# Optimization experiments

Hardware: AMD Instinct MI355X
Metric: run time of the kernel (lower is better)

## Reference

```python
import jax, jax.numpy as jnp
import numpy as np

D_MODEL = 512
NUM_HEADS = 8
D_HEAD = D_MODEL // NUM_HEADS


def setup_inputs() -> dict:
    key = jax.random.key(0)
    ks = jax.random.split(key, 9)
    B, L = 4, 2048
    s = 1.0 / np.sqrt(D_MODEL)
    inp = {
        "x": jax.random.normal(ks[0], (B, L, D_MODEL), dtype=jnp.float32),
        "Wq": jax.random.uniform(ks[1], (D_MODEL, D_MODEL), jnp.float32, -s, s),
        "bq": jax.random.uniform(ks[2], (D_MODEL,), jnp.float32, -s, s),
        "Wk": jax.random.uniform(ks[3], (D_MODEL, D_MODEL), jnp.float32, -s, s),
        "bk": jax.random.uniform(ks[4], (D_MODEL,), jnp.float32, -s, s),
        "Wv": jax.random.uniform(ks[5], (D_MODEL, D_MODEL), jnp.float32, -s, s),
        "bv": jax.random.uniform(ks[6], (D_MODEL,), jnp.float32, -s, s),
        "Wo": jax.random.uniform(ks[7], (D_MODEL, D_MODEL), jnp.float32, -s, s),
        "bo": jax.random.uniform(ks[8], (D_MODEL,), jnp.float32, -s, s),
    }
    return inp


def reference(x, Wq, bq, Wk, bk, Wv, bv, Wo, bo):
    B, L, _ = x.shape
    def split_heads(t):  # [B,L,D] -> [B,H,L,d]
        return t.reshape(B, L, NUM_HEADS, D_HEAD).transpose(0, 2, 1, 3)
    Q = split_heads(x @ Wq + bq)
    K = split_heads(x @ Wk + bk)
    V = split_heads(x @ Wv + bv)
    scale = 1.0 / jnp.sqrt(jnp.asarray(D_HEAD, dtype=x.dtype))
    scores = jnp.einsum('bhqd,bhkd->bhqk', Q, K) * scale  # [B,H,L,L]
    weights = jax.nn.softmax(scores, axis=-1)
    z = jnp.einsum('bhqk,bhkd->bhqd', weights, V)  # [B,H,L,d]
    z = z.transpose(0, 2, 1, 3).reshape(B, L, D_MODEL)
    return z @ Wo + bo
```

## Files before the change

### kernel.cpp

```cpp
#include <hip/hip_runtime.h>
#include <hip/hip_bf16.h>
#include <math.h>


#define MDIM 8192
#define DMODEL 512
#define NHEAD 8
#define DHEAD 64
#define LSEQ 2048

typedef __attribute__((ext_vector_type(8))) short short8;
typedef __attribute__((ext_vector_type(4))) float floatx4;

struct alignas(16) bf16x8 { __hip_bfloat16 v[8]; };
struct alignas(8)  bf16x4 { __hip_bfloat16 v[4]; };

__device__ __forceinline__ void load_lds16(const __hip_bfloat16* g, __hip_bfloat16* l) {
    __builtin_amdgcn_global_load_lds(
        (const __attribute__((address_space(1))) void*)g,
        (__attribute__((address_space(3))) void*)l,
        16, 0, 0);
}

__device__ __forceinline__ float fast_exp2(float x) {
#if __has_builtin(__builtin_amdgcn_exp2f)
    return __builtin_amdgcn_exp2f(x);
#else
    return __expf(x * 0.69314718055994531f);
#endif
}

__global__ __launch_bounds__(256) void cast_x_kernel(
    const float* __restrict__ x, __hip_bfloat16* __restrict__ xb)
{
    size_t i = ((size_t)blockIdx.x * 256 + threadIdx.x) * 8;
    float4 a = *reinterpret_cast<const float4*>(x + i);
    float4 b = *reinterpret_cast<const float4*>(x + i + 4);
    bf16x8 o;
    o.v[0] = __float2bfloat16(a.x); o.v[1] = __float2bfloat16(a.y);
    o.v[2] = __float2bfloat16(a.z); o.v[3] = __float2bfloat16(a.w);
    o.v[4] = __float2bfloat16(b.x); o.v[5] = __float2bfloat16(b.y);
    o.v[6] = __float2bfloat16(b.z); o.v[7] = __float2bfloat16(b.w);
    *reinterpret_cast<bf16x8*>(xb + i) = o;
}

__global__ __launch_bounds__(256) void transpose_cast_w(
    const float* __restrict__ Wq, const float* __restrict__ Wk,
    const float* __restrict__ Wv, const float* __restrict__ Wo,
    __hip_bfloat16* __restrict__ Wt)
{
    __shared__ float t[32][33];
    const int z = blockIdx.z;
    const float* W = z == 0 ? Wq : (z == 1 ? Wk : (z == 2 ? Wv : Wo));
    __hip_bfloat16* dst = Wt + ((size_t)z << 18);
    int k0 = blockIdx.x * 32, n0 = blockIdx.y * 32;
    int c = threadIdx.x & 31, r = threadIdx.x >> 5;
    #pragma unroll
    for (int i = 0; i < 4; ++i)
        t[r + 8 * i][c] = W[(size_t)(k0 + r + 8 * i) * DMODEL + n0 + c];
    __syncthreads();
    #pragma unroll
    for (int i = 0; i < 4; ++i)
        dst[(size_t)(n0 + r + 8 * i) * DMODEL + k0 + c] = __float2bfloat16(t[c][r + 8 * i]);
}

__global__ __launch_bounds__(256) void gemm_qkv_mfma(
    const __hip_bfloat16* __restrict__ xb,
    const __hip_bfloat16* __restrict__ Wt,
    const float* __restrict__ bq, const float* __restrict__ bk,
    const float* __restrict__ bv,
    __hip_bfloat16* __restrict__ Q2, __hip_bfloat16* __restrict__ K2,
    __hip_bfloat16* __restrict__ V2)
{
    __shared__ __hip_bfloat16 As[128 * 64];
    __shared__ __hip_bfloat16 Bs[128 * 64];

    const int tid = threadIdx.x;
    const int wid = tid >> 6, lane = tid & 63;
    const int l16 = lane & 15, quad = lane >> 4;
    const int wr = wid >> 1, wc = wid & 1;
    const int row0 = blockIdx.x * 128;
    const int which = blockIdx.y >> 2;
    const int col0 = (blockIdx.y & 3) * 128;
    const __hip_bfloat16* Wb = Wt + ((size_t)which << 18);
    const float* bias = which == 0 ? bq : (which == 1 ? bk : bv);

    const int r8 = lane >> 3, slot = lane & 7;
    const int cchunk = slot ^ (r8 & 7);

    floatx4 acc[4][4];
    #pragma unroll
    for (int i = 0; i < 4; ++i)
        #pragma unroll
        for (int j = 0; j < 4; ++j) acc[i][j] = floatx4{0.f, 0.f, 0.f, 0.f};

    for (int kt = 0; kt < DMODEL / 64; ++kt) {
        __syncthreads();
        #pragma unroll
        for (int j = 0; j < 4; ++j) {
            int seg = wid * 4 + j;
            int m = seg * 8 + r8;
            load_lds16(xb + (size_t)(row0 + m) * DMODEL + kt * 64 + cchunk * 8,
                       As + seg * 512);
            load_lds16(Wb + (size_t)(col0 + m) * DMODEL + kt * 64 + cchunk * 8,
                       Bs + seg * 512);
        }
        __syncthreads();

        #pragma unroll
        for (int ks = 0; ks < 2; ++ks) {
            const int c = ks * 4 + quad;
            short8 af[4], bf[4];
            #pragma unroll
            for (int mt = 0; mt < 4; ++mt) {
                int m = wr * 64 + mt * 16 + l16;
                af[mt] = *reinterpret_cast<const short8*>(As + m * 64 + ((c ^ (m & 7)) << 3));
            }
            #pragma unroll
            for (int nt = 0; nt < 4; ++nt) {
                int n = wc * 64 + nt * 16 + l16;
                bf[nt] = *reinterpret_cast<const short8*>(Bs + n * 64 + ((c ^ (n & 7)) << 3));
            }
            if (which < 2) {
                #pragma unroll
                for (int mt = 0; mt < 4; ++mt)
                    #pragma unroll
                    for (int nt = 0; nt < 4; ++nt)
                        acc[mt][nt] = __builtin_amdgcn_mfma_f32_16x16x32_bf16(
                            bf[nt], af[mt], acc[mt][nt], 0, 0, 0);
            } else {
                #pragma unroll
                for (int mt = 0; mt < 4; ++mt)
                    #pragma unroll
                    for (int nt = 0; nt < 4; ++nt)
                        acc[mt][nt] = __builtin_amdgcn_mfma_f32_16x16x32_bf16(
                            af[mt], bf[nt], acc[mt][nt], 0, 0, 0);
            }
        }
    }

    const float QSCALE = 0.18033688011112042f;

    if (which < 2) {
        __hip_bfloat16* dst = (which == 0) ? Q2 : K2;
        const float sc = (which == 0) ? QSCALE : 1.0f;
        #pragma unroll
        for (int mt = 0; mt < 4; ++mt) {
            const int mm = row0 + wr * 64 + mt * 16 + l16;
            const int b = mm >> 11, l = mm & 2047;
            int rowi;
            if (which == 0) {
                rowi = l;
            } else {
                int hi = l & ~127, w7 = l & 127;
                rowi = hi | (w7 & 96) | (((w7 >> 3) & 3) << 2)
                          | (((w7 >> 2) & 1) << 4) | (w7 & 3);
            }
            #pragma unroll
            for (int nt = 0; nt < 4; ++nt) {
                const int nnb = col0 + wc * 64 + nt * 16 + quad * 4;
                const float4 bv4 = *reinterpret_cast<const float4*>(&bias[nnb]);
                const int h = nnb >> 6, d = nnb & 63;
                const int s = d >> 5, q4 = (d >> 3) & 3, jb = d & 7;
                bf16x4 pk;
                pk.v[0] = __float2bfloat16((acc[mt][nt][0] + bv4.x) * sc);
                pk.v[1] = __float2bfloat16((acc[mt][nt][1] + bv4.y) * sc);
                pk.v[2] = __float2bfloat16((acc[mt][nt][2] + bv4.z) * sc);
                pk.v[3] = __float2bfloat16((acc[mt][nt][3] + bv4.w) * sc);
                size_t idx = ((((size_t)(b * NHEAD + h) * 128 + (rowi >> 4)) * 2 + s) << 9)
                             + q4 * 128 + (rowi & 15) * 8 + jb;
                *reinterpret_cast<bf16x4*>(dst + idx) = pk;
            }
        }
    } else {
        #pragma unroll
        for (int mt = 0; mt < 4; ++mt) {
            const int mmb = row0 + wr * 64 + mt * 16 + quad * 4;
            const int b = mmb >> 11, lb = mmb & 2047;
            #pragma unroll
            for (int nt = 0; nt < 4; ++nt) {
                const int nn = col0 + wc * 64 + nt * 16 + l16;
                const int h = nn >> 6, d = nn & 63;
                const float bv = bias[nn];
                bf16x4 pk;
                pk.v[0] = __float2bfloat16(acc[mt][nt][0] + bv);
                pk.v[1] = __float2bfloat16(acc[mt][nt][1] + bv);
                pk.v[2] = __float2bfloat16(acc[mt][nt][2] + bv);
                pk.v[3] = __float2bfloat16(acc[mt][nt][3] + bv);
                size_t idx = ((((size_t)(b * NHEAD + h) * 64 + (lb >> 5)) * 4 + (d >> 4)) << 9)
                             + ((lb >> 3) & 3) * 128 + (d & 15) * 8 + (lb & 7);
                *reinterpret_cast<bf16x4*>(V2 + idx) = pk;
            }
        }
    }
}

__global__ __launch_bounds__(256) void gemm_out_mfma(
    const __hip_bfloat16* __restrict__ Zb,
    const __hip_bfloat16* __restrict__ WoT,
    const float* __restrict__ bo, float* __restrict__ out)
{
    __shared__ __hip_bfloat16 As[128 * 64];
    __shared__ __hip_bfloat16 Bs[64 * 64];

    const int tid = threadIdx.x;
    const int wid = tid >> 6, lane = tid & 63;
    const int l16 = lane & 15, quad = lane >> 4;
    const int row0 = blockIdx.x * 128;
    const int col0 = blockIdx.y * 64;
    const int r8 = lane >> 3, slot = lane & 7;
    const int cchunk = slot ^ (r8 & 7);

    floatx4 acc[2][4];
    #pragma unroll
    for (int i = 0; i < 2; ++i)
        #pragma unroll
        for (int j = 0; j < 4; ++j) acc[i][j] = floatx4{0.f, 0.f, 0.f, 0.f};

    for (int kt = 0; kt < DMODEL / 64; ++kt) {
        __syncthreads();
        #pragma unroll
        for (int j = 0; j < 4; ++j) {
            int seg = wid * 4 + j;
            int m = seg * 8 + r8;
            load_lds16(Zb + (size_t)(row0 + m) * DMODEL + kt * 64 + cchunk * 8,
                       As + seg * 512);
        }
        #pragma unroll
        for (int j = 0; j < 2; ++j) {
            int seg = wid * 2 + j;
            int n = seg * 8 + r8;
            load_lds16(WoT + (size_t)(col0 + n) * DMODEL + kt * 64 + cchunk * 8,
                       Bs + seg * 512);
        }
        __syncthreads();

        #pragma unroll
        for (int ks = 0; ks < 2; ++ks) {
            const int c = ks * 4 + quad;
            short8 af[2], bf[4];
            #pragma unroll
            for (int mt = 0; mt < 2; ++mt) {
                int m = wid * 32 + mt * 16 + l16;
                af[mt] = *reinterpret_cast<const short8*>(As + m * 64 + ((c ^ (m & 7)) << 3));
            }
            #pragma unroll
            for (int nt = 0; nt < 4; ++nt) {
                int n = nt * 16 + l16;
                bf[nt] = *reinterpret_cast<const short8*>(Bs + n * 64 + ((c ^ (n & 7)) << 3));
            }
            #pragma unroll
            for (int mt = 0; mt < 2; ++mt)
                #pragma unroll
                for (int nt = 0; nt < 4; ++nt)
                    acc[mt][nt] = __builtin_amdgcn_mfma_f32_16x16x32_bf16(
                        af[mt], bf[nt], acc[mt][nt], 0, 0, 0);
        }
    }

    #pragma unroll
    for (int mt = 0; mt < 2; ++mt) {
        const int mmbase = row0 + wid * 32 + mt * 16 + quad * 4;
        #pragma unroll
        for (int nt = 0; nt < 4; ++nt) {
            const int nn = col0 + nt * 16 + l16;
            const float bias_v = bo[nn];
            #pragma unroll
            for (int r = 0; r < 4; ++r)
                out[(size_t)(mmbase + r) * DMODEL + nn] = acc[mt][nt][r] + bias_v;
        }
    }
}

__global__ __launch_bounds__(256) void attn_mfma(
    const __hip_bfloat16* __restrict__ Q2,
    const __hip_bfloat16* __restrict__ K2,
    const __hip_bfloat16* __restrict__ V2,
    __hip_bfloat16* __restrict__ Z)
{
    __shared__ float smem[4608];
    float* Lred = smem;
    float* Ored = smem + 256;

    const int bh = blockIdx.x & 31;
    const int qt = blockIdx.x >> 5;
    const int q0 = qt * 64;
    const int tid = threadIdx.x;
    const int wid = tid >> 6, lane = tid & 63;
    const int l16 = lane & 15, quad = lane >> 4;

    const __hip_bfloat16* Kc = K2 + (((size_t)bh * 128 * 2) << 9);
    const __hip_bfloat16* Vc = V2 + (((size_t)bh * 64 * 4) << 9);

    short8 qb[4][2];
    #pragma unroll
    for (int nt = 0; nt < 4; ++nt)
        #pragma unroll
        for (int s = 0; s < 2; ++s)
            qb[nt][s] = *reinterpret_cast<const short8*>(
                Q2 + ((((size_t)bh * 128 + qt * 4 + nt) * 2 + s) << 9) + lane * 8);

    floatx4 acc[4][4];
    #pragma unroll
    for (int i = 0; i < 4; ++i)
        #pragma unroll
        for (int j = 0; j < 4; ++j) acc[i][j] = floatx4{0.f, 0.f, 0.f, 0.f};
    float lsum[4] = {0.f, 0.f, 0.f, 0.f};

    short8 kb[2][2], vb[4];
    #pragma unroll
    for (int t = 0; t < 2; ++t)
        #pragma unroll
        for (int s = 0; s < 2; ++s)
            kb[t][s] = *reinterpret_cast<const short8*>(
                Kc + ((((size_t)(wid * 2 + t)) * 2 + s) << 9) + lane * 8);
    #pragma unroll
    for (int dt = 0; dt < 4; ++dt)
        vb[dt] = *reinterpret_cast<const short8*>(
            Vc + ((((size_t)wid) * 4 + dt) << 9) + lane * 8);

    for (int kt = 0; kt < LSEQ / 128; ++kt) {
        const int ktn = (kt + 1) & (LSEQ / 128 - 1);
        short8 nkb[2][2], nvb[4];
        #pragma unroll
        for (int t = 0; t < 2; ++t)
            #pragma unroll
            for (int s = 0; s < 2; ++s)
                nkb[t][s] = *reinterpret_cast<const short8*>(
                    Kc + ((((size_t)(ktn * 8 + wid * 2 + t)) * 2 + s) << 9) + lane * 8);
        #pragma unroll
        for (int dt = 0; dt < 4; ++dt)
            nvb[dt] = *reinterpret_cast<const short8*>(
                Vc + ((((size_t)(ktn * 4 + wid)) * 4 + dt) << 9) + lane * 8);

        floatx4 sacc[2][4];
        #pragma unroll
        for (int t = 0; t < 2; ++t)
            #pragma unroll
            for (int nt = 0; nt < 4; ++nt) sacc[t][nt] = floatx4{0.f, 0.f, 0.f, 0.f};
        #pragma unroll
        for (int s = 0; s < 2; ++s) {
            #pragma unroll
            for (int nt = 0; nt < 4; ++nt) {
                sacc[0][nt] = __builtin_amdgcn_mfma_f32_16x16x32_bf16(
                    kb[0][s], qb[nt][s], sacc[0][nt], 0, 0, 0);
                sacc[1][nt] = __builtin_amdgcn_mfma_f32_16x16x32_bf16(
                    kb[1][s], qb[nt][s], sacc[1][nt], 0, 0, 0);
            }
        }

        short8 pa[4];
        #pragma unroll
        for (int nt = 0; nt < 4; ++nt) {
            float e[8];
            #pragma unroll
            for (int t = 0; t < 2; ++t)
                #pragma unroll
                for (int r = 0; r < 4; ++r)
                    e[t * 4 + r] = fast_exp2(sacc[t][nt][r]);
            union { short8 s8; __hip_bfloat16 h[8]; } u;
            #pragma unroll
            for (int i = 0; i < 8; ++i) u.h[i] = __float2bfloat16(e[i]);
            lsum[nt] += ((e[0] + e[1]) + (e[2] + e[3])) + ((e[4] + e[5]) + (e[6] + e[7]));
            pa[nt] = u.s8;
        }

        #pragma unroll
        for (int dt = 0; dt < 4; ++dt)
            #pragma unroll
            for (int nt = 0; nt < 4; ++nt)
                acc[nt][dt] = __builtin_amdgcn_mfma_f32_16x16x32_bf16(
                    pa[nt], vb[dt], acc[nt][dt], 0, 0, 0);

        #pragma unroll
        for (int t = 0; t < 2; ++t)
            #pragma unroll
            for (int s = 0; s < 2; ++s) kb[t][s] = nkb[t][s];
        #pragma unroll
        for (int dt = 0; dt < 4; ++dt) vb[dt] = nvb[dt];
    }

    #pragma unroll
    for (int nt = 0; nt < 4; ++nt) {
        float v = lsum[nt];
        v += __shfl_xor(v, 16);
        v += __shfl_xor(v, 32);
        lsum[nt] = v;
    }
    if (quad == 0) {
        #pragma unroll
        for (int nt = 0; nt < 4; ++nt)
            Lred[wid * 64 + nt * 16 + l16] = lsum[nt];
    }

    const int b = bh >> 3, h = bh & 7;
    const int ql = tid >> 2;
    const int dg = tid & 3;
    float inv = 0.f;

    for (int dt = 0; dt < 4; ++dt) {
        __syncthreads();
        #pragma unroll
        for (int nt = 0; nt < 4; ++nt)
            *reinterpret_cast<floatx4*>(
                &Ored[(wid * 16 + l16) * 68 + nt * 16 + quad * 4]) = acc[nt][dt];
        __syncthreads();

        if (dt == 0)
            inv = 1.f / (Lred[ql] + Lred[64 + ql] + Lred[128 + ql] + Lred[192 + ql]);

        bf16x4 zo;
        #pragma unroll
        for (int i = 0; i < 4; ++i) {
            int d = dg * 4 + i;
            float ssum = Ored[d * 68 + ql] + Ored[(16 + d) * 68 + ql]
                       + Ored[(32 + d) * 68 + ql] + Ored[(48 + d) * 68 + ql];
            zo.v[i] = __float2bfloat16(ssum * inv);
        }
        *reinterpret_cast<bf16x4*>(
            Z + (size_t)(b * LSEQ + q0 + ql) * DMODEL + h * 64 + dt * 16 + dg * 4) = zo;
    }
}

extern "C" void kernel_launch(void* const* d_in, const int* in_sizes, int n_in,
                              void* d_out, int out_size, void* d_ws, size_t ws_size,
                              hipStream_t stream)
{
    const float* x  = (const float*)d_in[0];
    const float* Wq = (const float*)d_in[1]; const float* bq = (const float*)d_in[2];
    const float* Wk = (const float*)d_in[3]; const float* bk = (const float*)d_in[4];
    const float* Wv = (const float*)d_in[5]; const float* bv = (const float*)d_in[6];
    const float* Wo = (const float*)d_in[7]; const float* bo = (const float*)d_in[8];
    float* out = (float*)d_out;

    const size_t nqkv = (size_t)MDIM * DMODEL;
    __hip_bfloat16* xb = (__hip_bfloat16*)d_ws;
    __hip_bfloat16* Wt = xb + nqkv;
    __hip_bfloat16* Q2 = Wt + ((size_t)4 << 18);
    __hip_bfloat16* K2 = Q2 + nqkv;
    __hip_bfloat16* V2 = K2 + nqkv;
    __hip_bfloat16* Zb = V2 + nqkv;

    cast_x_kernel<<<dim3(MDIM * DMODEL / (256 * 8)), 256, 0, stream>>>(x, xb);
    transpose_cast_w<<<dim3(16, 16, 4), 256, 0, stream>>>(Wq, Wk, Wv, Wo, Wt);

    gemm_qkv_mfma<<<dim3(MDIM / 128, 12), 256, 0, stream>>>(
        xb, Wt, bq, bk, bv, Q2, K2, V2);

    attn_mfma<<<dim3(32 * (LSEQ / 64)), 256, 0, stream>>>(Q2, K2, V2, Zb);

    gemm_out_mfma<<<dim3(MDIM / 128, DMODEL / 64), 256, 0, stream>>>(
        Zb, Wt + ((size_t)3 << 18), bo, out);
}
```

Baseline: 159.6 us.

## Compute softmax row sums via MFMA with ones vector, drop register prefetch

Replaces the per-lane float accumulation of exp values and the cross-lane shuffle reduction with an extra MFMA that multiplies the bf16 probabilities by a ones vector, so the matrix unit produces the row sums. It also removes software double-buffering of the K/V fragments in favour of in-loop loads through incrementing pointers, and zero-initialises the score MFMAs through the accumulator operand. The changes cut VALU adds and register pressure but add MFMA work, expose global load latency without explicit prefetch, and sum the bf16-rounded probabilities instead of fp32 ones.

```diff
diff --git a/kernel.cpp b/kernel.cpp
--- a/kernel.cpp
+++ b/kernel.cpp
@@ -305,65 +305,65 @@
     for (int i = 0; i < 4; ++i)
         #pragma unroll
         for (int j = 0; j < 4; ++j) acc[i][j] = floatx4{0.f, 0.f, 0.f, 0.f};
-    float lsum[4] = {0.f, 0.f, 0.f, 0.f};
-
-    short8 kb[2][2], vb[4];
-    #pragma unroll
-    for (int t = 0; t < 2; ++t)
-        #pragma unroll
-        for (int s = 0; s < 2; ++s)
-            kb[t][s] = *reinterpret_cast<const short8*>(
-                Kc + ((((size_t)(wid * 2 + t)) * 2 + s) << 9) + lane * 8);
-    #pragma unroll
-    for (int dt = 0; dt < 4; ++dt)
-        vb[dt] = *reinterpret_cast<const short8*>(
-            Vc + ((((size_t)wid) * 4 + dt) << 9) + lane * 8);
+    floatx4 accl[4];
+    #pragma unroll
+    for (int i = 0; i < 4; ++i) accl[i] = floatx4{0.f, 0.f, 0.f, 0.f};
+
+    union { short8 s8; __hip_bfloat16 h[8]; } onesu;
+    #pragma unroll
+    for (int i = 0; i < 8; ++i) onesu.h[i] = __float2bfloat16(1.0f);
+    const short8 ones = onesu.s8;
+
+    const floatx4 fzero = floatx4{0.f, 0.f, 0.f, 0.f};
+
+    const __hip_bfloat16* kp = Kc + (((size_t)wid * 4) << 9) + lane * 8;
+    const __hip_bfloat16* vp = Vc + (((size_t)wid * 4) << 9) + lane * 8;
 
     for (int kt = 0; kt < LSEQ / 128; ++kt) {
-        const int ktn = (kt + 1) & (LSEQ / 128 - 1);
-        short8 nkb[2][2], nvb[4];
+        short8 kb[2][2], vb[4];
         #pragma unroll
         for (int t = 0; t < 2; ++t)
             #pragma unroll
             for (int s = 0; s < 2; ++s)
-                nkb[t][s] = *reinterpret_cast<const short8*>(
-                    Kc + ((((size_t)(ktn * 8 + wid * 2 + t)) * 2 + s) << 9) + lane * 8);
+                kb[t][s] = *reinterpret_cast<const short8*>(kp + ((t * 2 + s) << 9));
         #pragma unroll
         for (int dt = 0; dt < 4; ++dt)
-            nvb[dt] = *reinterpret_cast<const short8*>(
-                Vc + ((((size_t)(ktn * 4 + wid)) * 4 + dt) << 9) + lane * 8);
+            vb[dt] = *reinterpret_cast<const short8*>(vp + (dt << 9));
+        kp += (size_t)16 << 9;
+        vp += (size_t)16 << 9;
 
         floatx4 sacc[2][4];
         #pragma unroll
-        for (int t = 0; t < 2; ++t)
-            #pragma unroll
-            for (int nt = 0; nt < 4; ++nt) sacc[t][nt] = floatx4{0.f, 0.f, 0.f, 0.f};
-        #pragma unroll
-        for (int s = 0; s < 2; ++s) {
-            #pragma unroll
-            for (int nt = 0; nt < 4; ++nt) {
-                sacc[0][nt] = __builtin_amdgcn_mfma_f32_16x16x32_bf16(
-                    kb[0][s], qb[nt][s], sacc[0][nt], 0, 0, 0);
-                sacc[1][nt] = __builtin_amdgcn_mfma_f32_16x16x32_bf16(
-                    kb[1][s], qb[nt][s], sacc[1][nt], 0, 0, 0);
-            }
+        for (int nt = 0; nt < 4; ++nt) {
+            sacc[0][nt] = __builtin_amdgcn_mfma_f32_16x16x32_bf16(
+                kb[0][0], qb[nt][0], fzero, 0, 0, 0);
+            sacc[1][nt] = __builtin_amdgcn_mfma_f32_16x16x32_bf16(
+                kb[1][0], qb[nt][0], fzero, 0, 0, 0);
+        }
+        #pragma unroll
+        for (int nt = 0; nt < 4; ++nt) {
+            sacc[0][nt] = __builtin_amdgcn_mfma_f32_16x16x32_bf16(
+                kb[0][1], qb[nt][1], sacc[0][nt], 0, 0, 0);
+            sacc[1][nt] = __builtin_amdgcn_mfma_f32_16x16x32_bf16(
+                kb[1][1], qb[nt][1], sacc[1][nt], 0, 0, 0);
         }
 
         short8 pa[4];
         #pragma unroll
         for (int nt = 0; nt < 4; ++nt) {
-            float e[8];
+            union { short8 s8; __hip_bfloat16 h[8]; } u;
             #pragma unroll
             for (int t = 0; t < 2; ++t)
                 #pragma unroll
                 for (int r = 0; r < 4; ++r)
-                    e[t * 4 + r] = fast_exp2(sacc[t][nt][r]);
-            union { short8 s8; __hip_bfloat16 h[8]; } u;
-            #pragma unroll
-            for (int i = 0; i < 8; ++i) u.h[i] = __float2bfloat16(e[i]);
-            lsum[nt] += ((e[0] + e[1]) + (e[2] + e[3])) + ((e[4] + e[5]) + (e[6] + e[7]));
+                    u.h[t * 4 + r] = __float2bfloat16(fast_exp2(sacc[t][nt][r]));
             pa[nt] = u.s8;
         }
+
+        #pragma unroll
+        for (int nt = 0; nt < 4; ++nt)
+            accl[nt] = __builtin_amdgcn_mfma_f32_16x16x32_bf16(
+                pa[nt], ones, accl[nt], 0, 0, 0);
 
         #pragma unroll
         for (int dt = 0; dt < 4; ++dt)
@@ -371,26 +371,14 @@
             for (int nt = 0; nt < 4; ++nt)
                 acc[nt][dt] = __builtin_amdgcn_mfma_f32_16x16x32_bf16(
                     pa[nt], vb[dt], acc[nt][dt], 0, 0, 0);
-
-        #pragma unroll
-        for (int t = 0; t < 2; ++t)
-            #pragma unroll
-            for (int s = 0; s < 2; ++s) kb[t][s] = nkb[t][s];
-        #pragma unroll
-        for (int dt = 0; dt < 4; ++dt) vb[dt] = nvb[dt];
-    }
-
-    #pragma unroll
-    for (int nt = 0; nt < 4; ++nt) {
-        float v = lsum[nt];
-        v += __shfl_xor(v, 16);
-        v += __shfl_xor(v, 32);
-        lsum[nt] = v;
-    }
-    if (quad == 0) {
+    }
+
+    if (l16 == 0) {
         #pragma unroll
         for (int nt = 0; nt < 4; ++nt)
-            Lred[wid * 64 + nt * 16 + l16] = lsum[nt];
+            #pragma unroll
+            for (int r = 0; r < 4; ++r)
+                Lred[wid * 64 + nt * 16 + quad * 4 + r] = accl[nt][r];
     }
 
     const int b = bh >> 3, h = bh & 7;
```

New measurement: 158.6 us. About the same (-0.7%).
